# Optimization experiments

Hardware: AMD Instinct MI355X
Metric: run time of the kernel (lower is better)

## Reference

```python
import jax, jax.numpy as jnp
import numpy as np

H = 512

def setup_inputs() -> dict:
    key = jax.random.key(0)
    ks = jax.random.split(key, 10)
    T, B, S = 64, 8, 512
    scale = 1.0 / np.sqrt(H)
    return {
        "attn_dec_state": jax.random.normal(ks[0], (T, B, H), jnp.float32),
        "attn_enc_state": jax.random.normal(ks[1], (S, B, H), jnp.float32),
        "attn_coverage": jax.random.uniform(ks[2], (B, S), jnp.float32),
        "Wq": jax.random.normal(ks[3], (H, H), jnp.float32) * scale,   # linear_query weight (in,out)
        "bq": jnp.zeros((H,), jnp.float32),
        "Wc": jax.random.normal(ks[4], (H, H), jnp.float32) * scale,   # linear_context weight
        "v": jax.random.normal(ks[5], (H,), jnp.float32) * scale,       # v projection H->1
        "Wo": jax.random.normal(ks[6], (2 * H, H), jnp.float32) * scale,  # linear_out weight
        "bo": jnp.zeros((H,), jnp.float32),
        "wcov": jax.random.normal(ks[7], (H,), jnp.float32) * scale,    # linear_cover weight 1->H
    }

def reference(attn_dec_state, attn_enc_state, attn_coverage, Wq, bq, Wc, v, Wo, bo, wcov):
    dec = jnp.transpose(attn_dec_state, (1, 0, 2))   # [B,T,H]
    enc = jnp.transpose(attn_enc_state, (1, 0, 2))   # [B,S,H]
    # coverage: linear_cover(1->H) applied to each scalar, added to enc, then tanh
    enc = jnp.tanh(enc + attn_coverage[:, :, None] * wcov)  # [B,S,H]
    # additive (Bahdanau) score with broadcast-tanh
    a1 = jnp.einsum('bth,hk->btk', dec, Wq) + bq             # [B,T,H]
    a2 = jnp.einsum('bsh,hk->bsk', enc, Wc)                  # [B,S,H]
    scores = jnp.einsum('btsh,h->bts', jnp.tanh(a1[:, :, None, :] + a2[:, None, :, :]), v)  # [B,T,S]
    align = jax.nn.softmax(scores, axis=-1)                  # [B,T,S]
    c = jnp.einsum('bts,bsh->bth', align, enc)               # [B,T,H]
    concat = jnp.concatenate([c, dec], axis=-1)              # [B,T,2H]
    attn_h = jnp.einsum('btd,dk->btk', concat, Wo) + bo      # [B,T,H]
    attn_h = jnp.transpose(attn_h, (1, 0, 2))                # [T,B,H]
    align_out = jnp.transpose(align, (1, 0, 2))              # [T,B,S]
    return attn_h, align_out
```

## Files before the change

### kernel.cpp

```cpp
#include <hip/hip_runtime.h>
#include <cstddef>

static constexpr int TT = 64;
static constexpr int BB = 8;
static constexpr int SS = 512;
static constexpr int HH = 512;

typedef __attribute__((ext_vector_type(8))) short bf16x8;
typedef __attribute__((ext_vector_type(4))) float f32x4;

__device__ __forceinline__ float fast_tanh(float x) {
  float e = __expf(2.0f * x);
  return 1.0f - 2.0f * __builtin_amdgcn_rcpf(e + 1.0f);
}
__device__ __forceinline__ unsigned short f2bf(float f) {
  unsigned u = __float_as_uint(f);
  return (unsigned short)((u + 0x7FFFu + ((u >> 16) & 1u)) >> 16);
}

__global__ __launch_bounds__(256)
void k_prep(const float* __restrict__ enc, const float* __restrict__ cov,
            const float* __restrict__ wcov, const float* __restrict__ dec,
            const float* __restrict__ Wq, const float* __restrict__ Wc,
            const float* __restrict__ Wo, const float* __restrict__ v,
            const float* __restrict__ bo,
            unsigned short* __restrict__ encpb, unsigned short* __restrict__ decb,
            unsigned short* __restrict__ concatb,
            unsigned short* __restrict__ WqT, unsigned short* __restrict__ WcT,
            unsigned short* __restrict__ WoT,
            float* __restrict__ v2, float* __restrict__ Vsum,
            float* __restrict__ attn_h) {
  __shared__ float tile[32][33];
  const int blk = blockIdx.x, tid = threadIdx.x;

  if (blk < 8192) {
    const int idx = blk * 256 + tid;
    const int h = idx & 511;
    const int bs = idx >> 9;
    const int s = bs & 511, b = bs >> 9;
    const float x = enc[(size_t)(s * BB + b) * HH + h] + cov[bs] * wcov[h];
    encpb[idx] = f2bf(fast_tanh(x));
  } else if (blk < 9216) {
    const int idx = (blk - 8192) * 256 + tid;
    const int h = idx & 511, m = idx >> 9;
    const int b = m >> 6, t = m & 63;
    const unsigned short val = f2bf(dec[(size_t)(t * BB + b) * HH + h]);
    decb[idx] = val;
    concatb[(size_t)m * 1024 + 512 + h] = val;
  } else if (blk < 10240) {
    int l = blk - 9216;
    const float* W; unsigned short* WT; int KT;
    if (l < 256)      { W = Wq; WT = WqT; KT = 512; }
    else if (l < 512) { W = Wc; WT = WcT; KT = 512; l -= 256; }
    else              { W = Wo; WT = WoT; KT = 1024; l -= 512; }
    const int n0 = (l & 15) * 32, k0 = (l >> 4) * 32;
    const int r = tid >> 3, c4 = (tid & 7) * 4;
    const float4 w = *(const float4*)(W + (size_t)(k0 + r) * 512 + n0 + c4);
    tile[r][c4 + 0] = w.x; tile[r][c4 + 1] = w.y;
    tile[r][c4 + 2] = w.z; tile[r][c4 + 3] = w.w;
    __syncthreads();
    unsigned short* o = WT + (size_t)(n0 + r) * KT + k0 + c4;
#pragma unroll
    for (int i = 0; i < 4; ++i) o[i] = f2bf(tile[c4 + i][r]);
  } else if (blk == 10240) {
    __shared__ float rb[256];
    const float va = v[tid], vb = v[tid + 256];
    v2[tid] = 2.0f * va;
    v2[tid + 256] = 2.0f * vb;
    rb[tid] = va + vb;
    __syncthreads();
    for (int off = 128; off; off >>= 1) {
      if (tid < off) rb[tid] += rb[tid + off];
      __syncthreads();
    }
    if (tid == 0) Vsum[0] = rb[0];
  } else {
    const int row = blk - 10241;
    const float2 bv = *(const float2*)(bo + 2 * tid);
    *(float2*)(attn_h + (size_t)row * 512 + 2 * tid) = bv;
  }
}

template<int LDA, int LDB>
__device__ __forceinline__ void gemm_tile(const unsigned short* __restrict__ A,
                                          const unsigned short* __restrict__ BT,
                                          int m0, int n0, int kbeg, int kend,
                                          unsigned short (*As)[72],
                                          unsigned short (*Bs)[72],
                                          f32x4 acc[4]) {
  const int tid = threadIdx.x, w = tid >> 6, lane = tid & 63;
  const int lr = tid >> 2, lk = (tid & 3) * 16;
  const int fm = w * 16 + (lane & 15), fk = (lane >> 4) * 8;
  for (int k0 = kbeg; k0 < kend; k0 += 64) {
    const uint4* ga = (const uint4*)(A + (size_t)(m0 + lr) * LDA + k0 + lk);
    const uint4* gb = (const uint4*)(BT + (size_t)(n0 + lr) * LDB + k0 + lk);
    uint4 a0 = ga[0], a1 = ga[1], b0 = gb[0], b1 = gb[1];
    *(uint4*)&As[lr][lk] = a0;  *(uint4*)&As[lr][lk + 8] = a1;
    *(uint4*)&Bs[lr][lk] = b0;  *(uint4*)&Bs[lr][lk + 8] = b1;
    __syncthreads();
#pragma unroll
    for (int ks = 0; ks < 2; ++ks) {
      bf16x8 af = *(const bf16x8*)&As[fm][ks * 32 + fk];
#pragma unroll
      for (int j = 0; j < 4; ++j) {
        bf16x8 bf = *(const bf16x8*)&Bs[j * 16 + (lane & 15)][ks * 32 + fk];
        acc[j] = __builtin_amdgcn_mfma_f32_16x16x32_bf16(af, bf, acc[j], 0, 0, 0);
      }
    }
    __syncthreads();
  }
}

__global__ __launch_bounds__(256)
void k_gemm12(const unsigned short* __restrict__ decb,
              const unsigned short* __restrict__ encpb,
              const unsigned short* __restrict__ WqT,
              const unsigned short* __restrict__ WcT,
              const float* __restrict__ bq,
              float* __restrict__ Ea1, float* __restrict__ Ea2) {
  __shared__ unsigned short As[64][72];
  __shared__ unsigned short Bs[64][72];
  const int tid = threadIdx.x;
  const int w = tid >> 6, lane = tid & 63;

  const bool isA1 = blockIdx.x < 64;
  const int bb = isA1 ? blockIdx.x : blockIdx.x - 64;
  const int n0 = (bb & 7) * 64, m0 = (bb >> 3) * 64;
  const unsigned short* A  = isA1 ? decb : encpb;
  const unsigned short* BT = isA1 ? WqT : WcT;
  float* C = isA1 ? Ea1 : Ea2;

  f32x4 acc[4] = {};
  gemm_tile<512, 512>(A, BT, m0, n0, 0, 512, As, Bs, acc);

  const int col = lane & 15, rq = lane >> 4;
#pragma unroll
  for (int j = 0; j < 4; ++j) {
    const int n = n0 + j * 16 + col;
    const float bv = isA1 ? bq[n] : 0.0f;
#pragma unroll
    for (int r = 0; r < 4; ++r) {
      const int m = m0 + w * 16 + rq * 4 + r;
      float val = acc[j][r] + bv;
      val = fminf(fmaxf(val, -30.0f), 30.0f);
      C[(size_t)m * 512 + n] = __expf(2.0f * val);
    }
  }
}

__global__ __launch_bounds__(256)
void k_scores(const float* __restrict__ Ea1, const float* __restrict__ Ea2,
              const float* __restrict__ v2g, const float* __restrict__ Vsum,
              float* __restrict__ scb) {
  const int blk = blockIdx.x;
  const int b = blk & 7, tq = (blk >> 3) & 15, sh = blk >> 7;
  const int tid = threadIdx.x;
  const int wv = tid >> 6, lane = tid & 63;
  const int hq = lane & 3, sl = lane >> 2;

  __shared__ __align__(16) float ea1s[4][HH];
  __shared__ __align__(16) float v2s[HH];

#pragma unroll
  for (int i = 0; i < 4; ++i) {
    const float* row = Ea1 + (size_t)(b * TT + tq * 4 + i) * HH;
    ea1s[i][tid] = row[tid]; ea1s[i][tid + 256] = row[tid + 256];
  }
  v2s[tid] = v2g[tid]; v2s[tid + 256] = v2g[tid + 256];
  __syncthreads();

  const float V = Vsum[0];
  const int s0 = sh * 128 + wv * 32 + sl;
  const float* e2p0 = Ea2 + (size_t)(b * SS + s0) * HH;
  const float* e2p1 = e2p0 + (size_t)16 * HH;

  float acc[4][2] = {};
#define TERM(E1, E2, VV, A) A = fmaf(VV, __builtin_amdgcn_rcpf(fmaf(E1, E2, 1.0f)), A)
#pragma unroll 4
  for (int it = 0; it < 32; ++it) {
    const int h = it * 16 + hq * 4;
    const float4 e20 = *(const float4*)(e2p0 + h);
    const float4 e21 = *(const float4*)(e2p1 + h);
    const float4 vv  = *(const float4*)&v2s[h];
    float4 e1r[4];
    e1r[0] = *(const float4*)&ea1s[0][h];
    e1r[1] = *(const float4*)&ea1s[1][h];
    e1r[2] = *(const float4*)&ea1s[2][h];
    e1r[3] = *(const float4*)&ea1s[3][h];
#pragma unroll
    for (int i = 0; i < 4; ++i) {
      TERM(e1r[i].x, e20.x, vv.x, acc[i][0]);
      TERM(e1r[i].y, e20.y, vv.y, acc[i][0]);
      TERM(e1r[i].z, e20.z, vv.z, acc[i][0]);
      TERM(e1r[i].w, e20.w, vv.w, acc[i][0]);
      TERM(e1r[i].x, e21.x, vv.x, acc[i][1]);
      TERM(e1r[i].y, e21.y, vv.y, acc[i][1]);
      TERM(e1r[i].z, e21.z, vv.z, acc[i][1]);
      TERM(e1r[i].w, e21.w, vv.w, acc[i][1]);
    }
  }
#undef TERM
#pragma unroll
  for (int i = 0; i < 4; ++i) {
#pragma unroll
    for (int j = 0; j < 2; ++j) {
      acc[i][j] += __shfl_xor(acc[i][j], 1);
      acc[i][j] += __shfl_xor(acc[i][j], 2);
    }
  }
  if (hq == 0) {
#pragma unroll
    for (int i = 0; i < 4; ++i) {
#pragma unroll
      for (int j = 0; j < 2; ++j)
        scb[(size_t)(b * TT + tq * 4 + i) * SS + s0 + j * 16] = V - acc[i][j];
    }
  }
}

__global__ __launch_bounds__(256)
void k_smctx(const float* __restrict__ scb,
             const unsigned short* __restrict__ encpb,
             float* __restrict__ align_out,
             unsigned short* __restrict__ concatb) {
  const int b = blockIdx.x & 7;
  const int t0 = (blockIdx.x >> 3) * 2;
  const int tid = threadIdx.x;
  const int wave = tid >> 6, lane = tid & 63;

  __shared__ __align__(16) float al[2][SS];
  __shared__ float red[2][4];

  const float* r0 = scb + (size_t)(b * TT + t0) * SS;
  const float* r1 = r0 + SS;
  const float x00 = r0[tid], x01 = r0[tid + 256];
  const float x10 = r1[tid], x11 = r1[tid + 256];

  float m0 = fmaxf(x00, x01), m1 = fmaxf(x10, x11);
#pragma unroll
  for (int off = 32; off; off >>= 1) {
    m0 = fmaxf(m0, __shfl_xor(m0, off));
    m1 = fmaxf(m1, __shfl_xor(m1, off));
  }
  if (lane == 0) { red[0][wave] = m0; red[1][wave] = m1; }
  __syncthreads();
  m0 = fmaxf(fmaxf(red[0][0], red[0][1]), fmaxf(red[0][2], red[0][3]));
  m1 = fmaxf(fmaxf(red[1][0], red[1][1]), fmaxf(red[1][2], red[1][3]));
  __syncthreads();

  const float e00 = __expf(x00 - m0), e01 = __expf(x01 - m0);
  const float e10 = __expf(x10 - m1), e11 = __expf(x11 - m1);
  float s0 = e00 + e01, s1 = e10 + e11;
#pragma unroll
  for (int off = 32; off; off >>= 1) {
    s0 += __shfl_xor(s0, off);
    s1 += __shfl_xor(s1, off);
  }
  if (lane == 0) { red[0][wave] = s0; red[1][wave] = s1; }
  __syncthreads();
  s0 = red[0][0] + red[0][1] + red[0][2] + red[0][3];
  s1 = red[1][0] + red[1][1] + red[1][2] + red[1][3];
  const float rs0 = __builtin_amdgcn_rcpf(s0);
  const float rs1 = __builtin_amdgcn_rcpf(s1);

  const float a00 = e00 * rs0, a01 = e01 * rs0;
  const float a10 = e10 * rs1, a11 = e11 * rs1;
  float* ao0 = align_out + (size_t)(t0 + 0) * BB * SS + b * SS;
  float* ao1 = align_out + (size_t)(t0 + 1) * BB * SS + b * SS;
  ao0[tid] = a00; ao0[tid + 256] = a01;
  ao1[tid] = a10; ao1[tid + 256] = a11;
  al[0][tid] = a00; al[0][tid + 256] = a01;
  al[1][tid] = a10; al[1][tid + 256] = a11;
  __syncthreads();

  const unsigned* ep = (const unsigned*)(encpb + (size_t)b * SS * HH);
  float c00 = 0.f, c01 = 0.f, c10 = 0.f, c11 = 0.f;
#pragma unroll 16
  for (int s2 = 0; s2 < SS; ++s2) {
    const unsigned u = ep[s2 * 256 + tid];
    const float elo = __uint_as_float(u << 16);
    const float ehi = __uint_as_float(u & 0xffff0000u);
    const float av0 = al[0][s2], av1 = al[1][s2];
    c00 = fmaf(av0, elo, c00); c01 = fmaf(av0, ehi, c01);
    c10 = fmaf(av1, elo, c10); c11 = fmaf(av1, ehi, c11);
  }
  unsigned* cb0 = (unsigned*)(concatb + (size_t)(b * TT + t0) * 1024);
  unsigned* cb1 = (unsigned*)(concatb + (size_t)(b * TT + t0 + 1) * 1024);
  cb0[tid] = (unsigned)f2bf(c00) | ((unsigned)f2bf(c01) << 16);
  cb1[tid] = (unsigned)f2bf(c10) | ((unsigned)f2bf(c11) << 16);
}

__global__ __launch_bounds__(256)
void k_out(const unsigned short* __restrict__ A,
           const unsigned short* __restrict__ BT,
           float* __restrict__ C) {
  __shared__ unsigned short As[64][72];
  __shared__ unsigned short Bs[64][72];
  const int tid = threadIdx.x;
  const int w = tid >> 6, lane = tid & 63;
  const int tau = blockIdx.x >> 2, kc = blockIdx.x & 3;
  const int n0 = (tau & 7) * 64, m0 = (tau >> 3) * 64;

  f32x4 acc[4] = {};
  gemm_tile<1024, 1024>(A, BT, m0, n0, kc * 256, kc * 256 + 256, As, Bs, acc);

  const int col = lane & 15, rq = lane >> 4;
#pragma unroll
  for (int j = 0; j < 4; ++j) {
    const int n = n0 + j * 16 + col;
#pragma unroll
    for (int r = 0; r < 4; ++r) {
      const int m = m0 + w * 16 + rq * 4 + r;
      const int bi = m >> 6, t = m & 63;
      unsafeAtomicAdd(&C[(size_t)(t * BB + bi) * 512 + n], acc[j][r]);
    }
  }
}

extern "C" void kernel_launch(void* const* d_in, const int* in_sizes, int n_in,
                              void* d_out, int out_size, void* d_ws, size_t ws_size,
                              hipStream_t stream) {
  const float* dec  = (const float*)d_in[0];
  const float* enc  = (const float*)d_in[1];
  const float* cov  = (const float*)d_in[2];
  const float* Wq   = (const float*)d_in[3];
  const float* bq   = (const float*)d_in[4];
  const float* Wc   = (const float*)d_in[5];
  const float* v    = (const float*)d_in[6];
  const float* Wo   = (const float*)d_in[7];
  const float* bo   = (const float*)d_in[8];
  const float* wcov = (const float*)d_in[9];

  float* out = (float*)d_out;
  float* attn_h    = out;
  float* align_out = out + (size_t)TT * BB * HH;

  char* w = (char*)d_ws;
  const size_t MB = 1024 * 1024;
  unsigned short* encpb   = (unsigned short*)(w);
  unsigned short* WqT     = (unsigned short*)(w + 4 * MB);
  unsigned short* WcT     = (unsigned short*)(w + 5 * MB);
  unsigned short* WoT     = (unsigned short*)(w + 6 * MB);
  unsigned short* decb    = (unsigned short*)(w + 7 * MB);
  unsigned short* concatb = (unsigned short*)(w + 8 * MB);
  float*          Ea1     = (float*)(w + 9 * MB);
  float*          Ea2     = (float*)(w + 10 * MB);
  float*          scb     = (float*)(w + 18 * MB);
  float*          v2      = (float*)(w + 19 * MB);
  float*          Vsum    = (float*)(w + 19 * MB + 4096);

  k_prep<<<10753, 256, 0, stream>>>(enc, cov, wcov, dec, Wq, Wc, Wo, v, bo,
                                    encpb, decb, concatb, WqT, WcT, WoT,
                                    v2, Vsum, attn_h);
  k_gemm12<<<576, 256, 0, stream>>>(decb, encpb, WqT, WcT, bq, Ea1, Ea2);
  k_scores<<<512, 256, 0, stream>>>(Ea1, Ea2, v2, Vsum, scb);
  k_smctx<<<256, 256, 0, stream>>>(scb, encpb, align_out, concatb);
  k_out<<<256, 256, 0, stream>>>(concatb, WoT, attn_h);
}
```

Baseline: 144.0 us.

## Fuse scores, softmax and context into one kernel; fold decoder GEMM half into gemm12

The separate score and softmax/context kernels are merged into a single 512-thread kernel. It computes scores for two decoder steps over all encoder positions in shared memory, then runs softmax and the context reduction, so the score buffer no longer round-trips through global memory and one launch disappears. The decoder half of the output projection (with the bias) now runs inside the first GEMM kernel as extra blocks writing attn_h directly. This removes the separate bias initialisation, the decb copy and the v-preprocessing block, and the final kernel only atomically adds the context half. The catch: each fused block covers fewer time steps, so Ea2 is re-read by twice as many blocks, and the fused kernel has only 256 blocks.

```diff
diff --git a/kernel.cpp b/kernel.cpp
--- a/kernel.cpp
+++ b/kernel.cpp
@@ -22,14 +22,10 @@
 void k_prep(const float* __restrict__ enc, const float* __restrict__ cov,
             const float* __restrict__ wcov, const float* __restrict__ dec,
             const float* __restrict__ Wq, const float* __restrict__ Wc,
-            const float* __restrict__ Wo, const float* __restrict__ v,
-            const float* __restrict__ bo,
-            unsigned short* __restrict__ encpb, unsigned short* __restrict__ decb,
-            unsigned short* __restrict__ concatb,
+            const float* __restrict__ Wo,
+            unsigned short* __restrict__ encpb, unsigned short* __restrict__ concatb,
             unsigned short* __restrict__ WqT, unsigned short* __restrict__ WcT,
-            unsigned short* __restrict__ WoT,
-            float* __restrict__ v2, float* __restrict__ Vsum,
-            float* __restrict__ attn_h) {
+            unsigned short* __restrict__ WoT) {
   __shared__ float tile[32][33];
   const int blk = blockIdx.x, tid = threadIdx.x;
 
@@ -40,15 +36,13 @@
     const int s = bs & 511, b = bs >> 9;
     const float x = enc[(size_t)(s * BB + b) * HH + h] + cov[bs] * wcov[h];
     encpb[idx] = f2bf(fast_tanh(x));
-  } else if (blk < 9216) {
-    const int idx = (blk - 8192) * 256 + tid;
-    const int h = idx & 511, m = idx >> 9;
-    const int b = m >> 6, t = m & 63;
-    const unsigned short val = f2bf(dec[(size_t)(t * BB + b) * HH + h]);
-    decb[idx] = val;
-    concatb[(size_t)m * 1024 + 512 + h] = val;
-  } else if (blk < 10240) {
-    int l = blk - 9216;
+  } else if (blk < 8704) {
+    const int m = blk - 8192, t = m & 63, b = m >> 6;
+    const float2 dv = *(const float2*)(dec + (size_t)(t * BB + b) * HH + 2 * tid);
+    ((unsigned*)concatb)[(size_t)m * 512 + 256 + tid] =
+        (unsigned)f2bf(dv.x) | ((unsigned)f2bf(dv.y) << 16);
+  } else {
+    int l = blk - 8704;
     const float* W; unsigned short* WT; int KT;
     if (l < 256)      { W = Wq; WT = WqT; KT = 512; }
     else if (l < 512) { W = Wc; WT = WcT; KT = 512; l -= 256; }
@@ -62,22 +56,6 @@
     unsigned short* o = WT + (size_t)(n0 + r) * KT + k0 + c4;
 #pragma unroll
     for (int i = 0; i < 4; ++i) o[i] = f2bf(tile[c4 + i][r]);
-  } else if (blk == 10240) {
-    __shared__ float rb[256];
-    const float va = v[tid], vb = v[tid + 256];
-    v2[tid] = 2.0f * va;
-    v2[tid + 256] = 2.0f * vb;
-    rb[tid] = va + vb;
-    __syncthreads();
-    for (int off = 128; off; off >>= 1) {
-      if (tid < off) rb[tid] += rb[tid + off];
-      __syncthreads();
-    }
-    if (tid == 0) Vsum[0] = rb[0];
-  } else {
-    const int row = blk - 10241;
-    const float2 bv = *(const float2*)(bo + 2 * tid);
-    *(float2*)(attn_h + (size_t)row * 512 + 2 * tid) = bv;
   }
 }
 
@@ -112,182 +90,191 @@
 }
 
 __global__ __launch_bounds__(256)
-void k_gemm12(const unsigned short* __restrict__ decb,
+void k_gemm12(const unsigned short* __restrict__ concatb,
               const unsigned short* __restrict__ encpb,
               const unsigned short* __restrict__ WqT,
               const unsigned short* __restrict__ WcT,
-              const float* __restrict__ bq,
-              float* __restrict__ Ea1, float* __restrict__ Ea2) {
+              const unsigned short* __restrict__ WoT,
+              const float* __restrict__ bq, const float* __restrict__ bo,
+              float* __restrict__ Ea1, float* __restrict__ Ea2,
+              float* __restrict__ attn_h) {
   __shared__ unsigned short As[64][72];
   __shared__ unsigned short Bs[64][72];
-  const int tid = threadIdx.x;
+  const int g = blockIdx.x, tid = threadIdx.x;
   const int w = tid >> 6, lane = tid & 63;
-
-  const bool isA1 = blockIdx.x < 64;
-  const int bb = isA1 ? blockIdx.x : blockIdx.x - 64;
-  const int n0 = (bb & 7) * 64, m0 = (bb >> 3) * 64;
-  const unsigned short* A  = isA1 ? decb : encpb;
-  const unsigned short* BT = isA1 ? WqT : WcT;
-  float* C = isA1 ? Ea1 : Ea2;
-
-  f32x4 acc[4] = {};
-  gemm_tile<512, 512>(A, BT, m0, n0, 0, 512, As, Bs, acc);
-
   const int col = lane & 15, rq = lane >> 4;
-#pragma unroll
-  for (int j = 0; j < 4; ++j) {
-    const int n = n0 + j * 16 + col;
-    const float bv = isA1 ? bq[n] : 0.0f;
-#pragma unroll
-    for (int r = 0; r < 4; ++r) {
-      const int m = m0 + w * 16 + rq * 4 + r;
-      float val = acc[j][r] + bv;
-      val = fminf(fmaxf(val, -30.0f), 30.0f);
-      C[(size_t)m * 512 + n] = __expf(2.0f * val);
-    }
-  }
-}
-
-__global__ __launch_bounds__(256)
-void k_scores(const float* __restrict__ Ea1, const float* __restrict__ Ea2,
-              const float* __restrict__ v2g, const float* __restrict__ Vsum,
-              float* __restrict__ scb) {
-  const int blk = blockIdx.x;
-  const int b = blk & 7, tq = (blk >> 3) & 15, sh = blk >> 7;
-  const int tid = threadIdx.x;
+
+  if (g < 64) {
+    const int m0 = (g >> 3) * 64, n0 = (g & 7) * 64;
+    f32x4 acc[4] = {};
+    gemm_tile<1024, 512>(concatb + 512, WqT, m0, n0, 0, 512, As, Bs, acc);
+#pragma unroll
+    for (int j = 0; j < 4; ++j) {
+      const int n = n0 + j * 16 + col;
+      const float bv = bq[n];
+#pragma unroll
+      for (int r = 0; r < 4; ++r) {
+        const int m = m0 + w * 16 + rq * 4 + r;
+        float val = fminf(fmaxf(acc[j][r] + bv, -30.0f), 30.0f);
+        Ea1[(size_t)m * 512 + n] = __expf(2.0f * val);
+      }
+    }
+  } else if (g < 576) {
+    const int u = g - 64;
+    const int m0 = (u >> 3) * 64, n0 = (u & 7) * 64;
+    f32x4 acc[4] = {};
+    gemm_tile<512, 512>(encpb, WcT, m0, n0, 0, 512, As, Bs, acc);
+#pragma unroll
+    for (int j = 0; j < 4; ++j) {
+      const int n = n0 + j * 16 + col;
+#pragma unroll
+      for (int r = 0; r < 4; ++r) {
+        const int m = m0 + w * 16 + rq * 4 + r;
+        float val = fminf(fmaxf(acc[j][r], -30.0f), 30.0f);
+        Ea2[(size_t)m * 512 + n] = __expf(2.0f * val);
+      }
+    }
+  } else {
+    const int u = g - 576;
+    const int m0 = (u >> 3) * 64, n0 = (u & 7) * 64;
+    f32x4 acc[4] = {};
+    gemm_tile<1024, 1024>(concatb, WoT, m0, n0, 512, 1024, As, Bs, acc);
+#pragma unroll
+    for (int j = 0; j < 4; ++j) {
+      const int n = n0 + j * 16 + col;
+      const float bv = bo[n];
+#pragma unroll
+      for (int r = 0; r < 4; ++r) {
+        const int m = m0 + w * 16 + rq * 4 + r;
+        const int bi = m >> 6, t = m & 63;
+        attn_h[(size_t)(t * BB + bi) * 512 + n] = acc[j][r] + bv;
+      }
+    }
+  }
+}
+
+__global__ __launch_bounds__(512)
+void k_attn(const float* __restrict__ Ea1, const float* __restrict__ Ea2,
+            const float* __restrict__ v, const unsigned short* __restrict__ encpb,
+            float* __restrict__ align_out, unsigned short* __restrict__ concatb) {
+  __shared__ __align__(16) char smem[12352];
+  float (*sc)[512]   = (float(*)[512])smem;
+  float (*ea1s)[512] = (float(*)[512])(smem + 4096);
+  float* v2s         = (float*)(smem + 8192);
+  float2* part       = (float2*)(smem + 4096);
+  float (*red)[8]    = (float(*)[8])(smem + 12288);
+
+  const int g = blockIdx.x, tid = threadIdx.x;
+  const int b = g & 7, t0 = (g >> 3) * 2;
   const int wv = tid >> 6, lane = tid & 63;
   const int hq = lane & 3, sl = lane >> 2;
 
-  __shared__ __align__(16) float ea1s[4][HH];
-  __shared__ __align__(16) float v2s[HH];
-
-#pragma unroll
-  for (int i = 0; i < 4; ++i) {
-    const float* row = Ea1 + (size_t)(b * TT + tq * 4 + i) * HH;
-    ea1s[i][tid] = row[tid]; ea1s[i][tid + 256] = row[tid + 256];
-  }
-  v2s[tid] = v2g[tid]; v2s[tid + 256] = v2g[tid + 256];
-  __syncthreads();
-
-  const float V = Vsum[0];
-  const int s0 = sh * 128 + wv * 32 + sl;
-  const float* e2p0 = Ea2 + (size_t)(b * SS + s0) * HH;
-  const float* e2p1 = e2p0 + (size_t)16 * HH;
-
-  float acc[4][2] = {};
+  ea1s[0][tid] = Ea1[(size_t)(b * TT + t0) * HH + tid];
+  ea1s[1][tid] = Ea1[(size_t)(b * TT + t0 + 1) * HH + tid];
+  v2s[tid] = 2.0f * v[tid];
+  __syncthreads();
+
 #define TERM(E1, E2, VV, A) A = fmaf(VV, __builtin_amdgcn_rcpf(fmaf(E1, E2, 1.0f)), A)
+  for (int p = 0; p < 2; ++p) {
+    const int s0 = p * 256 + wv * 32 + sl;
+    const float* e2p0 = Ea2 + (size_t)(b * SS + s0) * HH;
+    const float* e2p1 = e2p0 + (size_t)16 * HH;
+    float acc[2][2] = {};
 #pragma unroll 4
-  for (int it = 0; it < 32; ++it) {
-    const int h = it * 16 + hq * 4;
-    const float4 e20 = *(const float4*)(e2p0 + h);
-    const float4 e21 = *(const float4*)(e2p1 + h);
-    const float4 vv  = *(const float4*)&v2s[h];
-    float4 e1r[4];
-    e1r[0] = *(const float4*)&ea1s[0][h];
-    e1r[1] = *(const float4*)&ea1s[1][h];
-    e1r[2] = *(const float4*)&ea1s[2][h];
-    e1r[3] = *(const float4*)&ea1s[3][h];
-#pragma unroll
-    for (int i = 0; i < 4; ++i) {
-      TERM(e1r[i].x, e20.x, vv.x, acc[i][0]);
-      TERM(e1r[i].y, e20.y, vv.y, acc[i][0]);
-      TERM(e1r[i].z, e20.z, vv.z, acc[i][0]);
-      TERM(e1r[i].w, e20.w, vv.w, acc[i][0]);
-      TERM(e1r[i].x, e21.x, vv.x, acc[i][1]);
-      TERM(e1r[i].y, e21.y, vv.y, acc[i][1]);
-      TERM(e1r[i].z, e21.z, vv.z, acc[i][1]);
-      TERM(e1r[i].w, e21.w, vv.w, acc[i][1]);
+    for (int it = 0; it < 32; ++it) {
+      const int h = it * 16 + hq * 4;
+      const float4 e20 = *(const float4*)(e2p0 + h);
+      const float4 e21 = *(const float4*)(e2p1 + h);
+      const float4 vvv = *(const float4*)&v2s[h];
+      float4 e1r[2];
+      e1r[0] = *(const float4*)&ea1s[0][h];
+      e1r[1] = *(const float4*)&ea1s[1][h];
+#pragma unroll
+      for (int i = 0; i < 2; ++i) {
+        TERM(e1r[i].x, e20.x, vvv.x, acc[i][0]);
+        TERM(e1r[i].y, e20.y, vvv.y, acc[i][0]);
+        TERM(e1r[i].z, e20.z, vvv.z, acc[i][0]);
+        TERM(e1r[i].w, e20.w, vvv.w, acc[i][0]);
+        TERM(e1r[i].x, e21.x, vvv.x, acc[i][1]);
+        TERM(e1r[i].y, e21.y, vvv.y, acc[i][1]);
+        TERM(e1r[i].z, e21.z, vvv.z, acc[i][1]);
+        TERM(e1r[i].w, e21.w, vvv.w, acc[i][1]);
+      }
+    }
+#pragma unroll
+    for (int i = 0; i < 2; ++i)
+#pragma unroll
+      for (int j = 0; j < 2; ++j) {
+        acc[i][j] += __shfl_xor(acc[i][j], 1);
+        acc[i][j] += __shfl_xor(acc[i][j], 2);
+      }
+    if (hq == 0) {
+      sc[0][s0] = -acc[0][0]; sc[0][s0 + 16] = -acc[0][1];
+      sc[1][s0] = -acc[1][0]; sc[1][s0 + 16] = -acc[1][1];
     }
   }
 #undef TERM
-#pragma unroll
-  for (int i = 0; i < 4; ++i) {
-#pragma unroll
-    for (int j = 0; j < 2; ++j) {
-      acc[i][j] += __shfl_xor(acc[i][j], 1);
-      acc[i][j] += __shfl_xor(acc[i][j], 2);
-    }
-  }
-  if (hq == 0) {
-#pragma unroll
-    for (int i = 0; i < 4; ++i) {
-#pragma unroll
-      for (int j = 0; j < 2; ++j)
-        scb[(size_t)(b * TT + tq * 4 + i) * SS + s0 + j * 16] = V - acc[i][j];
-    }
-  }
-}
-
-__global__ __launch_bounds__(256)
-void k_smctx(const float* __restrict__ scb,
-             const unsigned short* __restrict__ encpb,
-             float* __restrict__ align_out,
-             unsigned short* __restrict__ concatb) {
-  const int b = blockIdx.x & 7;
-  const int t0 = (blockIdx.x >> 3) * 2;
-  const int tid = threadIdx.x;
-  const int wave = tid >> 6, lane = tid & 63;
-
-  __shared__ __align__(16) float al[2][SS];
-  __shared__ float red[2][4];
-
-  const float* r0 = scb + (size_t)(b * TT + t0) * SS;
-  const float* r1 = r0 + SS;
-  const float x00 = r0[tid], x01 = r0[tid + 256];
-  const float x10 = r1[tid], x11 = r1[tid + 256];
-
-  float m0 = fmaxf(x00, x01), m1 = fmaxf(x10, x11);
+  __syncthreads();
+
+  const float x0 = sc[0][tid], x1 = sc[1][tid];
+  float m0 = x0, m1 = x1;
 #pragma unroll
   for (int off = 32; off; off >>= 1) {
     m0 = fmaxf(m0, __shfl_xor(m0, off));
     m1 = fmaxf(m1, __shfl_xor(m1, off));
   }
-  if (lane == 0) { red[0][wave] = m0; red[1][wave] = m1; }
-  __syncthreads();
-  m0 = fmaxf(fmaxf(red[0][0], red[0][1]), fmaxf(red[0][2], red[0][3]));
-  m1 = fmaxf(fmaxf(red[1][0], red[1][1]), fmaxf(red[1][2], red[1][3]));
-  __syncthreads();
-
-  const float e00 = __expf(x00 - m0), e01 = __expf(x01 - m0);
-  const float e10 = __expf(x10 - m1), e11 = __expf(x11 - m1);
-  float s0 = e00 + e01, s1 = e10 + e11;
+  if (lane == 0) { red[0][wv] = m0; red[1][wv] = m1; }
+  __syncthreads();
+  m0 = red[0][0]; m1 = red[1][0];
+#pragma unroll
+  for (int w2 = 1; w2 < 8; ++w2) { m0 = fmaxf(m0, red[0][w2]); m1 = fmaxf(m1, red[1][w2]); }
+  __syncthreads();
+  const float e0 = __expf(x0 - m0), e1 = __expf(x1 - m1);
+  float s0v = e0, s1v = e1;
 #pragma unroll
   for (int off = 32; off; off >>= 1) {
-    s0 += __shfl_xor(s0, off);
-    s1 += __shfl_xor(s1, off);
-  }
-  if (lane == 0) { red[0][wave] = s0; red[1][wave] = s1; }
-  __syncthreads();
-  s0 = red[0][0] + red[0][1] + red[0][2] + red[0][3];
-  s1 = red[1][0] + red[1][1] + red[1][2] + red[1][3];
-  const float rs0 = __builtin_amdgcn_rcpf(s0);
-  const float rs1 = __builtin_amdgcn_rcpf(s1);
-
-  const float a00 = e00 * rs0, a01 = e01 * rs0;
-  const float a10 = e10 * rs1, a11 = e11 * rs1;
-  float* ao0 = align_out + (size_t)(t0 + 0) * BB * SS + b * SS;
-  float* ao1 = align_out + (size_t)(t0 + 1) * BB * SS + b * SS;
-  ao0[tid] = a00; ao0[tid + 256] = a01;
-  ao1[tid] = a10; ao1[tid + 256] = a11;
-  al[0][tid] = a00; al[0][tid + 256] = a01;
-  al[1][tid] = a10; al[1][tid + 256] = a11;
-  __syncthreads();
-
-  const unsigned* ep = (const unsigned*)(encpb + (size_t)b * SS * HH);
-  float c00 = 0.f, c01 = 0.f, c10 = 0.f, c11 = 0.f;
-#pragma unroll 16
-  for (int s2 = 0; s2 < SS; ++s2) {
-    const unsigned u = ep[s2 * 256 + tid];
-    const float elo = __uint_as_float(u << 16);
-    const float ehi = __uint_as_float(u & 0xffff0000u);
-    const float av0 = al[0][s2], av1 = al[1][s2];
-    c00 = fmaf(av0, elo, c00); c01 = fmaf(av0, ehi, c01);
-    c10 = fmaf(av1, elo, c10); c11 = fmaf(av1, ehi, c11);
-  }
-  unsigned* cb0 = (unsigned*)(concatb + (size_t)(b * TT + t0) * 1024);
-  unsigned* cb1 = (unsigned*)(concatb + (size_t)(b * TT + t0 + 1) * 1024);
-  cb0[tid] = (unsigned)f2bf(c00) | ((unsigned)f2bf(c01) << 16);
-  cb1[tid] = (unsigned)f2bf(c10) | ((unsigned)f2bf(c11) << 16);
+    s0v += __shfl_xor(s0v, off);
+    s1v += __shfl_xor(s1v, off);
+  }
+  if (lane == 0) { red[0][wv] = s0v; red[1][wv] = s1v; }
+  __syncthreads();
+  float sum0 = 0.f, sum1 = 0.f;
+#pragma unroll
+  for (int w2 = 0; w2 < 8; ++w2) { sum0 += red[0][w2]; sum1 += red[1][w2]; }
+  const float a0 = e0 * __builtin_amdgcn_rcpf(sum0);
+  const float a1 = e1 * __builtin_amdgcn_rcpf(sum1);
+
+  align_out[(size_t)(t0 + 0) * BB * SS + b * SS + tid] = a0;
+  align_out[(size_t)(t0 + 1) * BB * SS + b * SS + tid] = a1;
+  sc[0][tid] = a0;
+  sc[1][tid] = a1;
+  __syncthreads();
+
+  {
+    const int sh = tid >> 8, hp = tid & 255;
+    const unsigned* ep = (const unsigned*)encpb + (size_t)b * SS * 256;
+    float c00 = 0.f, c01 = 0.f, c10 = 0.f, c11 = 0.f;
+#pragma unroll 8
+    for (int s2 = sh * 256; s2 < sh * 256 + 256; ++s2) {
+      const unsigned u = ep[s2 * 256 + hp];
+      const float elo = __uint_as_float(u << 16);
+      const float ehi = __uint_as_float(u & 0xffff0000u);
+      const float av0 = sc[0][s2], av1 = sc[1][s2];
+      c00 = fmaf(av0, elo, c00); c01 = fmaf(av0, ehi, c01);
+      c10 = fmaf(av1, elo, c10); c11 = fmaf(av1, ehi, c11);
+    }
+    part[(0 * 2 + sh) * 256 + hp] = make_float2(c00, c01);
+    part[(1 * 2 + sh) * 256 + hp] = make_float2(c10, c11);
+  }
+  __syncthreads();
+  {
+    const int t = tid >> 8, hp = tid & 255;
+    const float2 pa = part[(t * 2 + 0) * 256 + hp];
+    const float2 pb = part[(t * 2 + 1) * 256 + hp];
+    const float clo = pa.x + pb.x, chi = pa.y + pb.y;
+    ((unsigned*)concatb)[(size_t)(b * TT + t0 + t) * 512 + hp] =
+        (unsigned)f2bf(clo) | ((unsigned)f2bf(chi) << 16);
+  }
 }
 
 __global__ __launch_bounds__(256)
@@ -302,7 +289,7 @@
   const int n0 = (tau & 7) * 64, m0 = (tau >> 3) * 64;
 
   f32x4 acc[4] = {};
-  gemm_tile<1024, 1024>(A, BT, m0, n0, kc * 256, kc * 256 + 256, As, Bs, acc);
+  gemm_tile<1024, 1024>(A, BT, m0, n0, kc * 128, kc * 128 + 128, As, Bs, acc);
 
   const int col = lane & 15, rq = lane >> 4;
 #pragma unroll
@@ -339,21 +326,16 @@
   const size_t MB = 1024 * 1024;
   unsigned short* encpb   = (unsigned short*)(w);
   unsigned short* WqT     = (unsigned short*)(w + 4 * MB);
-  unsigned short* WcT     = (unsigned short*)(w + 5 * MB);
-  unsigned short* WoT     = (unsigned short*)(w + 6 * MB);
-  unsigned short* decb    = (unsigned short*)(w + 7 * MB);
-  unsigned short* concatb = (unsigned short*)(w + 8 * MB);
-  float*          Ea1     = (float*)(w + 9 * MB);
-  float*          Ea2     = (float*)(w + 10 * MB);
-  float*          scb     = (float*)(w + 18 * MB);
-  float*          v2      = (float*)(w + 19 * MB);
-  float*          Vsum    = (float*)(w + 19 * MB + 4096);
-
-  k_prep<<<10753, 256, 0, stream>>>(enc, cov, wcov, dec, Wq, Wc, Wo, v, bo,
-                                    encpb, decb, concatb, WqT, WcT, WoT,
-                                    v2, Vsum, attn_h);
-  k_gemm12<<<576, 256, 0, stream>>>(decb, encpb, WqT, WcT, bq, Ea1, Ea2);
-  k_scores<<<512, 256, 0, stream>>>(Ea1, Ea2, v2, Vsum, scb);
-  k_smctx<<<256, 256, 0, stream>>>(scb, encpb, align_out, concatb);
+  unsigned short* WcT     = (unsigned short*)(w + 4 * MB + 512 * 1024);
+  unsigned short* WoT     = (unsigned short*)(w + 5 * MB);
+  unsigned short* concatb = (unsigned short*)(w + 6 * MB);
+  float*          Ea1     = (float*)(w + 7 * MB);
+  float*          Ea2     = (float*)(w + 8 * MB);
+
+  k_prep<<<9728, 256, 0, stream>>>(enc, cov, wcov, dec, Wq, Wc, Wo,
+                                   encpb, concatb, WqT, WcT, WoT);
+  k_gemm12<<<640, 256, 0, stream>>>(concatb, encpb, WqT, WcT, WoT, bq, bo,
+                                    Ea1, Ea2, attn_h);
+  k_attn<<<256, 512, 0, stream>>>(Ea1, Ea2, v, encpb, align_out, concatb);
   k_out<<<256, 256, 0, stream>>>(concatb, WoT, attn_h);
 }
```

New measurement: 132.9 us. 1.08x faster.
